# Optimization experiments

Measured on AMD Instinct MI355X. Metric: run time of the kernel, lower is better.

Reference implementation:

```python
import jax, jax.numpy as jnp
import numpy as np

B, S, D, H = 2, 4096, 128, 128
EPS = 1e-6
NEG_INF = -1e30


def _complex_linear(xr, xi, Wr, Wi, br, bi):
    # x: (B,S,D); W: (H,D); complex linear (Wr + i Wi)(xr + i xi) + (br + i bi) per layer math:
    # real_out = (xr Wr + br) - (xi Wi + bi); imag_out = (xi Wr + br) + (xr Wi + bi)
    out_r = xr @ Wr.T + br - (xi @ Wi.T + bi)
    out_i = xi @ Wr.T + br + (xr @ Wi.T + bi)
    return out_r, out_i


def setup_inputs() -> dict:
    key = jax.random.key(0)
    ks = jax.random.split(key, 24)
    scale = 1.0 / np.sqrt(D)
    def W(k):
        return jax.random.normal(k, (H, D), jnp.float32) * scale
    def b(k):
        return jax.random.normal(k, (H,), jnp.float32) * 0.01
    inp = {
        "Z_q": jax.random.normal(ks[0], (B, 2, S, D, 1), jnp.float32),
        "Z_k": jax.random.normal(ks[1], (B, 2, S, D, 1), jnp.float32),
        "Z_v": jax.random.normal(ks[2], (B, 2, S, D, 1), jnp.float32),
        "Wq_r": W(ks[3]), "Wq_i": W(ks[4]), "bq_r": b(ks[5]), "bq_i": b(ks[6]),
        "Wk_r": W(ks[7]), "Wk_i": W(ks[8]), "bk_r": b(ks[9]), "bk_i": b(ks[10]),
        "Wv_r": W(ks[11]), "Wv_i": W(ks[12]), "bv_r": b(ks[13]), "bv_i": b(ks[14]),
        "Wp_r": W(ks[15]), "Wp_i": W(ks[16]), "bp_r": b(ks[17]), "bp_i": b(ks[18]),
        "noise_floor": jnp.asarray(1.0, jnp.float32),
        "tau": jnp.asarray(0.0, jnp.float32),
    }
    return inp


def reference(Z_q, Z_k, Z_v,
              Wq_r, Wq_i, bq_r, bq_i,
              Wk_r, Wk_i, bk_r, bk_i,
              Wv_r, Wv_i, bv_r, bv_i,
              Wp_r, Wp_i, bp_r, bp_i,
              noise_floor, tau):
    # squeeze trailing singleton; split real/imag -> (B,S,D)
    zqr, zqi = Z_q[:, 0, :, :, 0], Z_q[:, 1, :, :, 0]
    zkr, zki = Z_k[:, 0, :, :, 0], Z_k[:, 1, :, :, 0]
    zvr, zvi = Z_v[:, 0, :, :, 0], Z_v[:, 1, :, :, 0]

    Qr, Qi = _complex_linear(zqr, zqi, Wq_r, Wq_i, bq_r, bq_i)
    Kr, Ki = _complex_linear(zkr, zki, Wk_r, Wk_i, bk_r, bk_i)
    Vr, Vi = _complex_linear(zvr, zvi, Wv_r, Wv_i, bv_r, bv_i)

    # InverseMahalanobis: R2[b,i,j] = sum_h |Q[b,i]-K[b,j]|^2
    q2 = jnp.sum(Qr * Qr + Qi * Qi, axis=-1)          # (B,S)
    k2 = jnp.sum(Kr * Kr + Ki * Ki, axis=-1)          # (B,S)
    re_qk = (jnp.einsum('bsh,bth->bst', Qr, Kr)
             + jnp.einsum('bsh,bth->bst', Qi, Ki))    # (B,S,S)
    R2 = q2[:, :, None] + k2[:, None, :] - 2.0 * re_qk

    attn_scores = -jax.nn.softplus(tau) * jnp.log(noise_floor ** 2 + R2 + EPS)
    mask = jnp.tril(jnp.ones((S, S), dtype=bool))[None]
    attn_scores = jnp.where(mask, attn_scores, NEG_INF)
    attn_weights = jax.nn.softmax(attn_scores / jnp.sqrt(jnp.float32(H)), axis=-1)

    # attn (real) times complex V
    est_r = jnp.einsum('bst,bth->bsh', attn_weights, Vr)
    est_i = jnp.einsum('bst,bth->bsh', attn_weights, Vi)

    out_r, out_i = _complex_linear(est_r, est_i, Wp_r, Wp_i, bp_r, bp_i)
    out = jnp.stack((out_r, out_i), axis=1)[..., None]  # (B,2,S,H,1)
    return out, attn_weights
```

## Files before the change

### kernel.cpp

```cpp
#include <hip/hip_runtime.h>

#define S_LEN 4096
#define OUT_ELEMS 2097152

typedef _Float16 f16;
typedef _Float16 f16x8 __attribute__((ext_vector_type(8)));
typedef _Float16 f16x4 __attribute__((ext_vector_type(4)));
typedef float f32x4 __attribute__((ext_vector_type(4)));

#define MT_OFF    0x000000
#define BIAS_OFF  0x080000
#define SC_OFF    0x081000
#define QH_OFF    0x100000
#define KH_OFF    0x500000
#define VH_OFF    0x900000
#define Q2_OFF    0xD00000
#define K2_OFF    0xD10000
#define L_OFF     0xD20000
#define VPT_OFF   0xE00000
#define PW_OFF    0x1600000
#define WS_NEED   0x5600000

#define MFMA16(A,B,C) __builtin_amdgcn_mfma_f32_16x16x32_f16(A,B,C,0,0,0)

__device__ __forceinline__ void async_cp16(f16* lds, const f16* g) {
  __builtin_amdgcn_global_load_lds(
      (const __attribute__((address_space(1))) void*)g,
      (__attribute__((address_space(3))) void*)lds, 16, 0, 0);
}


template<int LC>
__device__ __forceinline__ void stageT(f16* lds, const f16* g, size_t stride, int tid) {
#pragma unroll
  for (int i = 0; i < (1 << (LC - 1)); ++i) {
    int idx = i*256 + tid;
    int row = idx >> LC, c = idx & ((1 << LC) - 1);
    int cl = c ^ (row & 7);
    async_cp16(lds + idx*8, g + (size_t)row*stride + cl*8);
  }
}

template<int LC>
__device__ __forceinline__ void mfma_stepT(const f16* Asm, const f16* Bsm, int kb,
                                           int lane, int wm, int wn, f32x4 acc[4][4]) {
  f16x8 a[4], b[4];
  int rr = lane & 15, q = lane >> 4;
  int L = kb*4 + q;
#pragma unroll
  for (int i=0;i<4;i++) {
    int row = wm + i*16 + rr;
    a[i] = *(const f16x8*)(Asm + (row << (LC+3)) + ((L ^ (row & 7)) << 3));
  }
#pragma unroll
  for (int j=0;j<4;j++) {
    int row = wn + j*16 + rr;
    b[j] = *(const f16x8*)(Bsm + (row << (LC+3)) + ((L ^ (row & 7)) << 3));
  }
#pragma unroll
  for (int i=0;i<4;i++)
#pragma unroll
    for (int j=0;j<4;j++) acc[i][j] = MFMA16(a[i], b[j], acc[i][j]);
}

__device__ __forceinline__ void stage16(f16* lds, const f16* g, int stride, int tid) {
#pragma unroll
  for (int i = 0; i < 2; ++i) {
    int idx = i*256 + tid;
    int row = idx >> 2, c = idx & 3;
    int cs = c ^ ((row >> 1) & 3);
    async_cp16(lds + idx*8, g + (size_t)row*stride + cs*8);
  }
}

__device__ __forceinline__ void mfma_step(const f16* Asm, const f16* Bsm, int lane,
                                          int wm, int wn, f32x4 acc[4][4]) {
  f16x8 a[4], b[4];
  int rr = lane & 15;
  int sc = (lane >> 4) ^ ((rr >> 1) & 3);
#pragma unroll
  for (int i=0;i<4;i++) a[i] = *(const f16x8*)(Asm + (wm + i*16 + rr)*32 + (sc<<3));
#pragma unroll
  for (int j=0;j<4;j++) b[j] = *(const f16x8*)(Bsm + (wn + j*16 + rr)*32 + (sc<<3));
#pragma unroll
  for (int i=0;i<4;i++)
#pragma unroll
    for (int j=0;j<4;j++) acc[i][j] = MFMA16(a[i], b[j], acc[i][j]);
}

__global__ __launch_bounds__(256)
void k_build(const float* Wqr, const float* Wqi, const float* bqr, const float* bqi,
             const float* Wkr, const float* Wki, const float* bkr, const float* bki,
             const float* Wvr, const float* Wvi, const float* bvr, const float* bvi,
             const float* Wpr, const float* Wpi, const float* bpr, const float* bpi,
             f16* Mt, float* bias) {
  int mat = blockIdx.x;
  const float *Wr, *Wi, *br, *bi;
  if (mat == 0)      { Wr=Wqr; Wi=Wqi; br=bqr; bi=bqi; }
  else if (mat == 1) { Wr=Wkr; Wi=Wki; br=bkr; bi=bki; }
  else if (mat == 2) { Wr=Wvr; Wi=Wvi; br=bvr; bi=bvi; }
  else               { Wr=Wpr; Wi=Wpi; br=bpr; bi=bpi; }
  int idx = blockIdx.y*256 + threadIdx.x;
  int n = idx >> 8, k = idx & 255;
  int d = k & 127, h = n & 127;
  float w = (k < 128) ? ((n < 128) ? Wr[h*128+d] : Wi[h*128+d])
                      : ((n < 128) ? -Wi[h*128+d] : Wr[h*128+d]);
  Mt[mat*65536 + n*256 + k] = (f16)w;
  if (k == 0)
    bias[mat*256 + n] = (n < 128) ? (br[n] - bi[n]) : (br[n-128] + bi[n-128]);
}

__global__ __launch_bounds__(256)
void k_init(float* attn, float* zreg, float* sc, const float* nf, const float* tau) {
  int bx = blockIdx.x, tid = threadIdx.x;
  float4 z = make_float4(0.f,0.f,0.f,0.f);
  if (bx < 992) {
    int b = bx >= 496; int r = bx - b*496;
    int tb = 1; while (r >= tb) { r -= tb; tb++; }
    int sb = r;
    float* base = attn + ((size_t)(b*S_LEN) + sb*128)*S_LEN + tb*128;
    int c4 = tid & 31;
#pragma unroll
    for (int it = 0; it < 16; ++it) {
      int row = it*8 + (tid >> 5);
      *(float4*)(base + (size_t)row*S_LEN + c4*4) = z;
    }
    return;
  }
  int idx = (bx - 992)*256 + tid;
  if (idx < 12288) ((float4*)zreg)[idx] = z;
  if (idx == 0) {
    float t = tau[0];
    float c = __builtin_log2f(1.0f + __builtin_exp2f(t * 1.4426950408889634f))
              * 0.6931471805599453f;
    sc[0] = -c * 0.08838834764831845f;
    sc[1] = nf[0]*nf[0] + 1e-6f;
  }
}

__global__ __launch_bounds__(256)
void k_proj(const float* Zq, const float* Zk, const float* Zv,
            const f16* Mt, const float* bias,
            f16* Qh, f16* Kh, f16* Vh, float* q2, float* k2) {
  __shared__ f16 Asm[128*256];
  __shared__ f16 Bsm[128*256];
  __shared__ float bias_s[128];
  int tid = threadIdx.x;
  int mode = blockIdx.z;
  int m0 = blockIdx.x * 128, n0 = blockIdx.y * 128;
  const float* Z = (mode==0) ? Zq : (mode==1 ? Zk : Zv);
  if (tid < 128) bias_s[tid] = bias[mode*256 + n0 + tid];
  int b = m0 >> 12, s0 = m0 & 4095;
  stageT<5>(Bsm, Mt + mode*65536 + n0*256, 256, tid);
  const float* Zb = Z + ((size_t)(b*2))*S_LEN*128 + (size_t)s0*128;
#pragma unroll
  for (int i = 0; i < 32; ++i) {
    int idx = i*256 + tid;
    int row = idx >> 6, c4 = idx & 63;
    int part = c4 >> 5, d4 = c4 & 31;
    float4 v = *(const float4*)(Zb + ((size_t)part*S_LEN + row)*128 + d4*4);
    f16x4 hv; hv[0]=(f16)v.x; hv[1]=(f16)v.y; hv[2]=(f16)v.z; hv[3]=(f16)v.w;
    int ch = c4 >> 1;
    *(f16x4*)(Asm + (row << 8) + ((ch ^ (row & 7)) << 3) + (c4 & 1)*4) = hv;
  }
  __syncthreads();
  int lane = tid & 63, w = tid >> 6;
  int wm = (w >> 1)*64, wn = (w & 1)*64;
  f32x4 acc[4][4] = {};
#pragma unroll
  for (int kb = 0; kb < 8; ++kb) mfma_stepT<5>(Asm, Bsm, kb, lane, wm, wn, acc);
  int rr = (lane>>4)*4, cc = lane & 15;
  f16* O = (mode==0) ? Qh : (mode==1 ? Kh : Vh);
  float rs[4][4];
#pragma unroll
  for (int i=0;i<4;i++)
#pragma unroll
    for (int r=0;r<4;r++) rs[i][r]=0.f;
#pragma unroll
  for (int i=0;i<4;i++)
#pragma unroll
    for (int j=0;j<4;j++) {
      int cl = wn + j*16 + cc;
      int cg = n0 + cl;
      float bv = bias_s[cl];
#pragma unroll
      for (int r=0;r<4;r++) {
        int rg = m0 + wm + i*16 + rr + r;
        f16 hv = (f16)(acc[i][j][r] + bv);
        O[(size_t)rg*256 + cg] = hv;
        float fv = (float)hv;
        rs[i][r] += fv*fv;
      }
    }
  if (mode < 2) {
#pragma unroll
    for (int m=8;m>=1;m>>=1)
#pragma unroll
      for (int i=0;i<4;i++)
#pragma unroll
        for (int r=0;r<4;r++) rs[i][r] += __shfl_xor(rs[i][r], m, 64);
    if (cc == 0) {
      float* T = (mode==0) ? q2 : k2;
#pragma unroll
      for (int i=0;i<4;i++)
#pragma unroll
        for (int r=0;r<4;r++) {
          int rg = m0 + wm + i*16 + rr + r;
          atomicAdd(&T[rg], rs[i][r]);
        }
    }
  }
}

__global__ __launch_bounds__(256)
void k_vp(const f16* Vh, const f16* Mt, f16* VPt) {
  __shared__ f16 Asm[2][128*32];
  __shared__ f16 Bsm[2][128*32];
  int t0 = blockIdx.x*128, n0 = blockIdx.y*128, b = blockIdx.z;
  int tid = threadIdx.x;
  int lane = tid & 63, w = tid >> 6;
  int wm = (w>>1)*64, wn = (w&1)*64;
  const f16* Ag = Mt + 3*65536 + n0*256;
  const f16* Bg = Vh + ((size_t)(b*S_LEN) + t0)*256;
  f32x4 acc[4][4] = {};
  stage16(Asm[0], Ag, 256, tid);
  stage16(Bsm[0], Bg, 256, tid);
  __syncthreads();
  for (int kb=0;kb<8;kb++) {
    int cur = kb & 1;
    if (kb < 7) {
      stage16(Asm[cur^1], Ag + (kb+1)*32, 256, tid);
      stage16(Bsm[cur^1], Bg + (kb+1)*32, 256, tid);
    }
    mfma_step(Asm[cur], Bsm[cur], lane, wm, wn, acc);
    __syncthreads();
  }
  int rr = (lane>>4)*4, cc = lane & 15;
#pragma unroll
  for (int i=0;i<4;i++) {
    int n = n0 + wm + i*16 + rr;
#pragma unroll
    for (int j=0;j<4;j++) {
      int t = t0 + wn + j*16 + cc;
#pragma unroll
      for (int r=0;r<4;r++)
        VPt[(size_t)b*1048576 + (size_t)(n + r)*4096 + t] = (f16)acc[i][j][r];
    }
  }
}

__global__ __launch_bounds__(256)
void k_attn(const f16* Qh, const f16* Kh, const float* q2, const float* k2,
            const float* sc, float* lsum, f16* Pws) {
  __shared__ f16 Qs[128*256];
  __shared__ f16 Ks[128*256];
  __shared__ float q2s[128], k2s[128];
  int x = blockIdx.x;
  int b = x >= 528; int r = x - b*528;
  int sb = 0; while (r > sb) { r -= sb + 1; sb++; }
  int tb = r;
  int s0 = sb*128, t0 = tb*128;
  int tid = threadIdx.x;
  stageT<5>(Qs, Qh + ((size_t)(b*S_LEN) + s0)*256, 256, tid);
  stageT<5>(Ks, Kh + ((size_t)(b*S_LEN) + t0)*256, 256, tid);
  if (tid < 128) {
    q2s[tid] = q2[b*S_LEN + s0 + tid];
    k2s[tid] = k2[b*S_LEN + t0 + tid];
  }
  __syncthreads();
  float kc = sc[0], nf2 = sc[1];
  int lane = tid & 63, w = tid >> 6;
  int wm = (w >> 1)*64, wn = (w & 1)*64;
  f32x4 acc[4][4] = {};
#pragma unroll
  for (int kb = 0; kb < 8; ++kb) mfma_stepT<5>(Qs, Ks, kb, lane, wm, wn, acc);
  int rr = (lane>>4)*4, cc = lane & 15;
  bool diag = (tb == sb);
  float rs[4][4];
#pragma unroll
  for (int i=0;i<4;i++)
#pragma unroll
    for (int rg=0;rg<4;rg++) rs[i][rg]=0.f;
#pragma unroll
  for (int i=0;i<4;i++)
#pragma unroll
    for (int j=0;j<4;j++) {
      int cl = wn + j*16 + cc;
      float kv = k2s[cl];
#pragma unroll
      for (int rg=0;rg<4;rg++) {
        int rl = wm + i*16 + rr + rg;
        float xx = nf2 + q2s[rl] + kv - 2.0f*acc[i][j][rg];
        float P = __builtin_exp2f(kc * __builtin_log2f(__builtin_fmaxf(xx, 1e-6f)));
        if (diag && (t0+cl) > (s0+rl)) P = 0.f;
        Pws[((size_t)(b*S_LEN) + s0 + rl)*S_LEN + t0 + cl] = (f16)P;
        rs[i][rg] += P;
      }
    }
#pragma unroll
  for (int m=8;m>=1;m>>=1)
#pragma unroll
    for (int i=0;i<4;i++)
#pragma unroll
      for (int rg=0;rg<4;rg++) rs[i][rg] += __shfl_xor(rs[i][rg], m, 64);
  if (cc == 0)
#pragma unroll
    for (int i=0;i<4;i++)
#pragma unroll
      for (int rg=0;rg<4;rg++) {
        int rl = wm + i*16 + rr + rg;
        atomicAdd(&lsum[b*S_LEN + s0 + rl], rs[i][rg]);
      }
}

__global__ __launch_bounds__(256)
void k_pv(const f16* Pws, const f16* VPt, const float* lsum, const float* bias,
          float* outp, float* attn) {
  __shared__ f16 Asm[2][128*128];
  __shared__ f16 Bsm[2][128*128];
  __shared__ float ls[128];
  __shared__ float bias_s[128];
  int sb = blockIdx.x, nb = blockIdx.y, b = blockIdx.z;
  int s0 = sb*128, h0 = nb*128;
  int nt = sb + 1;
  int tid = threadIdx.x;
  bool wrb = (nb == 0);
  if (tid < 128) {
    ls[tid] = 1.0f / lsum[b*S_LEN + s0 + tid];
    bias_s[tid] = bias[3*256 + h0 + tid];
  }
  const f16* Abase = Pws + ((size_t)(b*S_LEN) + s0)*S_LEN;
  const f16* Bbase = VPt + (size_t)b*1048576 + (size_t)h0*4096;
  stageT<4>(Asm[0], Abase, S_LEN, tid);
  stageT<4>(Bsm[0], Bbase, 4096, tid);
  __syncthreads();
  int lane = tid & 63, w = tid >> 6;
  int wm = (w>>1)*64, wn = (w&1)*64;
  f32x4 acc[4][4] = {};
  for (int t = 0; t < nt; ++t) {
    int cur = t & 1;
    if (t + 1 < nt) {
      stageT<4>(Asm[cur^1], Abase + (t+1)*128, S_LEN, tid);
      stageT<4>(Bsm[cur^1], Bbase + (t+1)*128, 4096, tid);
    }
    if (wrb) {
      int c4 = tid & 31;
#pragma unroll
      for (int i = 0; i < 16; ++i) {
        int idx = i*256 + tid;
        int row = idx >> 5;
        float invl = ls[row];
        f16x4 v = *(const f16x4*)(Asm[cur] + (row << 7)
                                  + (((c4 >> 1) ^ (row & 7)) << 3) + (c4 & 1)*4);
        float4 o;
        o.x=(float)v[0]*invl; o.y=(float)v[1]*invl; o.z=(float)v[2]*invl; o.w=(float)v[3]*invl;
        *(float4*)(attn + ((size_t)(b*S_LEN) + s0 + row)*S_LEN + t*128 + c4*4) = o;
      }
    }
#pragma unroll
    for (int kb = 0; kb < 4; ++kb) mfma_stepT<4>(Asm[cur], Bsm[cur], kb, lane, wm, wn, acc);
    __syncthreads();
  }
  int rr = (lane>>4)*4, cc = lane & 15;
#pragma unroll
  for (int i=0;i<4;i++)
#pragma unroll
    for (int j=0;j<4;j++) {
      int cl = wn + j*16 + cc;
      int cg = h0 + cl;
      int comp = cg >> 7, h = cg & 127;
      float bv = bias_s[cl];
#pragma unroll
      for (int rg=0;rg<4;rg++) {
        int rl = wm + i*16 + rr + rg;
        outp[(((size_t)(b*2 + comp))*S_LEN + s0 + rl)*128 + h] = acc[i][j][rg]*ls[rl] + bv;
      }
    }
}

extern "C" void kernel_launch(void* const* d_in, const int* in_sizes, int n_in,
                              void* d_out, int out_size, void* d_ws, size_t ws_size,
                              hipStream_t stream) {
  (void)in_sizes; (void)n_in; (void)out_size;
  if (ws_size < (size_t)WS_NEED) return;
  const float* Zq = (const float*)d_in[0];
  const float* Zk = (const float*)d_in[1];
  const float* Zv = (const float*)d_in[2];
  char* ws = (char*)d_ws;
  f16*   Mt   = (f16*)(ws + MT_OFF);
  float* bias = (float*)(ws + BIAS_OFF);
  float* sc   = (float*)(ws + SC_OFF);
  f16*   Qh   = (f16*)(ws + QH_OFF);
  f16*   Kh   = (f16*)(ws + KH_OFF);
  f16*   Vh   = (f16*)(ws + VH_OFF);
  float* q2   = (float*)(ws + Q2_OFF);
  float* k2   = (float*)(ws + K2_OFF);
  float* lsum = (float*)(ws + L_OFF);
  f16*   VPt  = (f16*)(ws + VPT_OFF);
  f16*   Pws  = (f16*)(ws + PW_OFF);
  float* outp = (float*)d_out;
  float* attn = outp + OUT_ELEMS;

  k_build<<<dim3(4,256), 256, 0, stream>>>(
      (const float*)d_in[3],  (const float*)d_in[4],  (const float*)d_in[5],  (const float*)d_in[6],
      (const float*)d_in[7],  (const float*)d_in[8],  (const float*)d_in[9],  (const float*)d_in[10],
      (const float*)d_in[11], (const float*)d_in[12], (const float*)d_in[13], (const float*)d_in[14],
      (const float*)d_in[15], (const float*)d_in[16], (const float*)d_in[17], (const float*)d_in[18],
      Mt, bias);
  k_init<<<1040, 256, 0, stream>>>(attn, q2, sc, (const float*)d_in[19], (const float*)d_in[20]);
  k_proj<<<dim3(64,2,3), 256, 0, stream>>>(Zq, Zk, Zv, Mt, bias, Qh, Kh, Vh, q2, k2);
  k_vp<<<dim3(32,2,2), 256, 0, stream>>>(Vh, Mt, VPt);
  k_attn<<<1056, 256, 0, stream>>>(Qh, Kh, q2, k2, sc, lsum, Pws);
  k_pv<<<dim3(32,2,2), 256, 0, stream>>>(Pws, VPt, lsum, bias, outp, attn);
}
```

Before: 343.5 us.

## Recompute attention probabilities in PV kernel instead of materializing them

The fp16 probability matrix is no longer written to workspace. A new k_lsum kernel computes only the row sums of the scores. k_pv recomputes the Q·K scores per key block, writes the normalized attention output, and multiplies by VP in a split-K layout over groups of up to four key blocks. Outputs are accumulated with atomics onto an output buffer that k_init now pre-fills with the bias. The projection epilogue also stages results through LDS so the global stores are coalesced. This removes a large round trip of the intermediate matrix and raises the block count in the PV stage, at the cost of computing QK twice and adding float atomics.

After: 402.6 us. 1.17x slower.

```diff
diff --git a/kernel.cpp b/kernel.cpp
--- a/kernel.cpp
+++ b/kernel.cpp
@@ -18,7 +18,6 @@
 #define K2_OFF    0xD10000
 #define L_OFF     0xD20000
 #define VPT_OFF   0xE00000
-#define PW_OFF    0x1600000
 #define WS_NEED   0x5600000
 
 #define MFMA16(A,B,C) __builtin_amdgcn_mfma_f32_16x16x32_f16(A,B,C,0,0,0)
@@ -111,7 +110,8 @@
 }
 
 __global__ __launch_bounds__(256)
-void k_init(float* attn, float* zreg, float* sc, const float* nf, const float* tau) {
+void k_init(float* outp, float* attn, float* zreg, float* sc, const float* bias,
+            const float* nf, const float* tau) {
   int bx = blockIdx.x, tid = threadIdx.x;
   float4 z = make_float4(0.f,0.f,0.f,0.f);
   if (bx < 992) {
@@ -128,7 +128,14 @@
     return;
   }
   int idx = (bx - 992)*256 + tid;
-  if (idx < 12288) ((float4*)zreg)[idx] = z;
+  if (idx < 524288) {
+    int h4 = idx & 31;
+    int comp = (idx >> 17) & 1;
+    ((float4*)outp)[idx] = *(const float4*)(bias + 3*256 + comp*128 + h4*4);
+  } else {
+    int j = idx - 524288;
+    if (j < 12288) ((float4*)zreg)[j] = z;
+  }
   if (idx == 0) {
     float t = tau[0];
     float c = __builtin_log2f(1.0f + __builtin_exp2f(t * 1.4426950408889634f))
@@ -169,8 +176,10 @@
   f32x4 acc[4][4] = {};
 #pragma unroll
   for (int kb = 0; kb < 8; ++kb) mfma_stepT<5>(Asm, Bsm, kb, lane, wm, wn, acc);
-  int rr = (lane>>4)*4, cc = lane & 15;
+  int rr2 = (lane>>4)*4, cc = lane & 15;
   f16* O = (mode==0) ? Qh : (mode==1 ? Kh : Vh);
+  __syncthreads();
+  f16* Osm = Asm;
   float rs[4][4];
 #pragma unroll
   for (int i=0;i<4;i++)
@@ -181,17 +190,23 @@
 #pragma unroll
     for (int j=0;j<4;j++) {
       int cl = wn + j*16 + cc;
-      int cg = n0 + cl;
       float bv = bias_s[cl];
 #pragma unroll
       for (int r=0;r<4;r++) {
-        int rg = m0 + wm + i*16 + rr + r;
+        int rl = wm + i*16 + rr2 + r;
         f16 hv = (f16)(acc[i][j][r] + bv);
-        O[(size_t)rg*256 + cg] = hv;
+        Osm[rl*128 + cl] = hv;
         float fv = (float)hv;
         rs[i][r] += fv*fv;
       }
     }
+  __syncthreads();
+#pragma unroll
+  for (int i2 = 0; i2 < 8; ++i2) {
+    int idx = i2*256 + tid;
+    int row = idx >> 4, c = idx & 15;
+    *(f16x8*)(O + (size_t)(m0+row)*256 + n0 + c*8) = *(const f16x8*)(Osm + row*128 + c*8);
+  }
   if (mode < 2) {
 #pragma unroll
     for (int m=8;m>=1;m>>=1)
@@ -205,7 +220,7 @@
       for (int i=0;i<4;i++)
 #pragma unroll
         for (int r=0;r<4;r++) {
-          int rg = m0 + wm + i*16 + rr + r;
+          int rg = m0 + wm + i*16 + rr2 + r;
           atomicAdd(&T[rg], rs[i][r]);
         }
     }
@@ -235,10 +250,10 @@
     mfma_step(Asm[cur], Bsm[cur], lane, wm, wn, acc);
     __syncthreads();
   }
-  int rr = (lane>>4)*4, cc = lane & 15;
+  int rr2 = (lane>>4)*4, cc = lane & 15;
 #pragma unroll
   for (int i=0;i<4;i++) {
-    int n = n0 + wm + i*16 + rr;
+    int n = n0 + wm + i*16 + rr2;
 #pragma unroll
     for (int j=0;j<4;j++) {
       int t = t0 + wn + j*16 + cc;
@@ -249,9 +264,9 @@
   }
 }
 
-__global__ __launch_bounds__(256)
-void k_attn(const f16* Qh, const f16* Kh, const float* q2, const float* k2,
-            const float* sc, float* lsum, f16* Pws) {
+__global__ __launch_bounds__(512, 2)
+void k_lsum(const f16* Qh, const f16* Kh, const float* q2, const float* k2,
+            const float* sc, float* lsum) {
   __shared__ f16 Qs[128*256];
   __shared__ f16 Ks[128*256];
   __shared__ float q2s[128], k2s[128];
@@ -261,20 +276,35 @@
   int tb = r;
   int s0 = sb*128, t0 = tb*128;
   int tid = threadIdx.x;
-  stageT<5>(Qs, Qh + ((size_t)(b*S_LEN) + s0)*256, 256, tid);
-  stageT<5>(Ks, Kh + ((size_t)(b*S_LEN) + t0)*256, 256, tid);
-  if (tid < 128) {
-    q2s[tid] = q2[b*S_LEN + s0 + tid];
-    k2s[tid] = k2[b*S_LEN + t0 + tid];
-  }
+  const f16* Qg = Qh + ((size_t)(b*S_LEN) + s0)*256;
+  const f16* Kg = Kh + ((size_t)(b*S_LEN) + t0)*256;
+#pragma unroll
+  for (int i=0;i<8;i++) {
+    int idx = i*512 + tid, row = idx >> 5, c = idx & 31, cl = c ^ (row & 7);
+    async_cp16(Qs + idx*8, Qg + (size_t)row*256 + cl*8);
+    async_cp16(Ks + idx*8, Kg + (size_t)row*256 + cl*8);
+  }
+  if (tid < 128) { q2s[tid]=q2[b*S_LEN+s0+tid]; k2s[tid]=k2[b*S_LEN+t0+tid]; }
   __syncthreads();
   float kc = sc[0], nf2 = sc[1];
   int lane = tid & 63, w = tid >> 6;
-  int wm = (w >> 1)*64, wn = (w & 1)*64;
-  f32x4 acc[4][4] = {};
-#pragma unroll
-  for (int kb = 0; kb < 8; ++kb) mfma_stepT<5>(Qs, Ks, kb, lane, wm, wn, acc);
-  int rr = (lane>>4)*4, cc = lane & 15;
+  int wm = (w>>2)*64, wn = (w&3)*32;
+  int rr = lane & 15, qq = lane >> 4;
+  f32x4 acc[4][2] = {};
+#pragma unroll
+  for (int kb=0;kb<8;kb++) {
+    int L = kb*4 + qq;
+    f16x8 a[4], bb[2];
+#pragma unroll
+    for (int i=0;i<4;i++){ int row=wm+i*16+rr; a[i]=*(const f16x8*)(Qs + row*256 + ((L^(row&7))<<3)); }
+#pragma unroll
+    for (int j=0;j<2;j++){ int row=wn+j*16+rr; bb[j]=*(const f16x8*)(Ks + row*256 + ((L^(row&7))<<3)); }
+#pragma unroll
+    for (int i=0;i<4;i++)
+#pragma unroll
+      for (int j=0;j<2;j++) acc[i][j]=MFMA16(a[i],bb[j],acc[i][j]);
+  }
+  int rr2 = qq*4, cc = rr;
   bool diag = (tb == sb);
   float rs[4][4];
 #pragma unroll
@@ -284,16 +314,15 @@
 #pragma unroll
   for (int i=0;i<4;i++)
 #pragma unroll
-    for (int j=0;j<4;j++) {
+    for (int j=0;j<2;j++) {
       int cl = wn + j*16 + cc;
       float kv = k2s[cl];
 #pragma unroll
       for (int rg=0;rg<4;rg++) {
-        int rl = wm + i*16 + rr + rg;
+        int rl = wm + i*16 + rr2 + rg;
         float xx = nf2 + q2s[rl] + kv - 2.0f*acc[i][j][rg];
         float P = __builtin_exp2f(kc * __builtin_log2f(__builtin_fmaxf(xx, 1e-6f)));
         if (diag && (t0+cl) > (s0+rl)) P = 0.f;
-        Pws[((size_t)(b*S_LEN) + s0 + rl)*S_LEN + t0 + cl] = (f16)P;
         rs[i][rg] += P;
       }
     }
@@ -307,73 +336,152 @@
 #pragma unroll
     for (int i=0;i<4;i++)
 #pragma unroll
+      for (int rg=0;rg<4;rg++)
+        atomicAdd(&lsum[b*S_LEN + s0 + wm + i*16 + rr2 + rg], rs[i][rg]);
+}
+
+__global__ __launch_bounds__(512, 2)
+void k_pv(const f16* Qh, const f16* Kh, const f16* VPt,
+          const float* q2, const float* k2, const float* sc,
+          const float* lsum, float* outp, float* attn) {
+  __shared__ f16 Qs[128*256];
+  __shared__ f16 KPV[128*256];
+  int r = blockIdx.x, b = blockIdx.y;
+  int sb = 0; while (r >= ((sb+4)>>2)) { r -= (sb+4)>>2; sb++; }
+  int c = r;
+  int s0 = sb*128;
+  int tid = threadIdx.x;
+  int lane = tid & 63, w = tid >> 6;
+  int wm = (w>>2)*64;
+  int wnq = (w&3)*32;
+  int wnp = (w&3)*64;
+  int rr = lane & 15, qq = lane >> 4, rr2 = qq*4, cc = rr;
+  const f16* Qg = Qh + ((size_t)(b*S_LEN) + s0)*256;
+#pragma unroll
+  for (int i=0;i<8;i++) {
+    int idx = i*512 + tid, row = idx >> 5, ch = idx & 31, cl = ch ^ (row & 7);
+    async_cp16(Qs + idx*8, Qg + (size_t)row*256 + cl*8);
+  }
+  float kc = sc[0], nf2 = sc[1];
+  float q2v[4][4], lsr[4][4];
+#pragma unroll
+  for (int i=0;i<4;i++) {
+    float4 qv = *(const float4*)(q2  + b*S_LEN + s0 + wm + i*16 + rr2);
+    float4 lv = *(const float4*)(lsum + b*S_LEN + s0 + wm + i*16 + rr2);
+    q2v[i][0]=qv.x; q2v[i][1]=qv.y; q2v[i][2]=qv.z; q2v[i][3]=qv.w;
+    lsr[i][0]=1.0f/lv.x; lsr[i][1]=1.0f/lv.y; lsr[i][2]=1.0f/lv.z; lsr[i][3]=1.0f/lv.w;
+  }
+  float invl[8];
+#pragma unroll
+  for (int i=0;i<8;i++) { int row=(i*512+tid)>>5; invl[i]=1.0f/lsum[b*S_LEN+s0+row]; }
+  const f16* VPg = VPt + (size_t)b*1048576;
+  f32x4 pacc[4][4] = {};
+  int tb0 = c*4, tb1 = tb0 + 4; if (tb1 > sb+1) tb1 = sb+1;
+  for (int tb = tb0; tb < tb1; ++tb) {
+    int t0 = tb*128;
+    bool diag = (tb == sb);
+    __syncthreads();
+    const f16* Kg = Kh + ((size_t)(b*S_LEN) + t0)*256;
+#pragma unroll
+    for (int i=0;i<8;i++) {
+      int idx = i*512 + tid, row = idx >> 5, ch = idx & 31, cl = ch ^ (row & 7);
+      async_cp16(KPV + idx*8, Kg + (size_t)row*256 + cl*8);
+    }
+    __syncthreads();
+    f32x4 qacc[4][2] = {};
+#pragma unroll
+    for (int kb=0;kb<8;kb++) {
+      int L = kb*4 + qq;
+      f16x8 a[4], bb[2];
+#pragma unroll
+      for (int i=0;i<4;i++){ int row=wm+i*16+rr; a[i]=*(const f16x8*)(Qs + row*256 + ((L^(row&7))<<3)); }
+#pragma unroll
+      for (int j=0;j<2;j++){ int row=wnq+j*16+rr; bb[j]=*(const f16x8*)(KPV + row*256 + ((L^(row&7))<<3)); }
+#pragma unroll
+      for (int i=0;i<4;i++)
+#pragma unroll
+        for (int j=0;j<2;j++) qacc[i][j]=MFMA16(a[i],bb[j],qacc[i][j]);
+    }
+    __syncthreads();
+#pragma unroll
+    for (int i=0;i<4;i++) {
+      int idx = i*512 + tid, row = idx >> 3, ch = idx & 7, cl = ch ^ (row & 7);
+      async_cp16(KPV + 16384 + idx*8, VPg + (size_t)row*4096 + t0 + cl*8);
+    }
+    float kv2[2];
+#pragma unroll
+    for (int j=0;j<2;j++) kv2[j] = k2[b*S_LEN + t0 + wnq + j*16 + cc];
+#pragma unroll
+    for (int i=0;i<4;i++)
+#pragma unroll
+      for (int j=0;j<2;j++) {
+        int cl = wnq + j*16 + cc;
+#pragma unroll
+        for (int rg=0;rg<4;rg++) {
+          int rl = wm + i*16 + rr2 + rg;
+          float xx = nf2 + q2v[i][rg] + kv2[j] - 2.0f*qacc[i][j][rg];
+          float P = __builtin_exp2f(kc * __builtin_log2f(__builtin_fmaxf(xx, 1e-6f)));
+          if (diag && (t0+cl) > (s0+rl)) P = 0.f;
+          int ch = cl >> 3;
+          KPV[rl*128 + ((ch ^ (rl&7)) << 3) + (cl & 7)] = (f16)P;
+        }
+      }
+    __syncthreads();
+#pragma unroll
+    for (int i2=0;i2<8;i2++) {
+      int idx = i2*512 + tid, row = idx >> 5, c4 = idx & 31;
+      f16x4 v = *(const f16x4*)(KPV + row*128 + (((c4>>1) ^ (row&7)) << 3) + (c4&1)*4);
+      float4 o;
+      o.x=(float)v[0]*invl[i2]; o.y=(float)v[1]*invl[i2];
+      o.z=(float)v[2]*invl[i2]; o.w=(float)v[3]*invl[i2];
+      *(float4*)(attn + ((size_t)(b*S_LEN) + s0 + row)*S_LEN + t0 + c4*4) = o;
+    }
+#pragma unroll
+    for (int kk=0;kk<2;kk++) {
+      int Lp = kk*4 + qq;
+      f16x8 a[4], bb[4];
+#pragma unroll
+      for (int i=0;i<4;i++){ int row=wm+i*16+rr; a[i]=*(const f16x8*)(KPV + row*128 + ((Lp^(row&7))<<3)); }
+#pragma unroll
+      for (int j=0;j<4;j++){ int rv=wnp+j*16+rr; bb[j]=*(const f16x8*)(KPV + 16384 + rv*64 + ((Lp^(rv&7))<<3)); }
+#pragma unroll
+      for (int i=0;i<4;i++)
+#pragma unroll
+        for (int j=0;j<4;j++) pacc[i][j]=MFMA16(a[i],bb[j],pacc[i][j]);
+    }
+    __syncthreads();
+#pragma unroll
+    for (int i=0;i<4;i++) {
+      int idx = i*512 + tid, row = idx >> 3, ch = idx & 7, cl = ch ^ (row & 7);
+      async_cp16(KPV + 16384 + idx*8, VPg + (size_t)row*4096 + t0 + 64 + cl*8);
+    }
+    __syncthreads();
+#pragma unroll
+    for (int kk=0;kk<2;kk++) {
+      int Lp = 8 + kk*4 + qq;
+      int Lv = kk*4 + qq;
+      f16x8 a[4], bb[4];
+#pragma unroll
+      for (int i=0;i<4;i++){ int row=wm+i*16+rr; a[i]=*(const f16x8*)(KPV + row*128 + ((Lp^(row&7))<<3)); }
+#pragma unroll
+      for (int j=0;j<4;j++){ int rv=wnp+j*16+rr; bb[j]=*(const f16x8*)(KPV + 16384 + rv*64 + ((Lv^(rv&7))<<3)); }
+#pragma unroll
+      for (int i=0;i<4;i++)
+#pragma unroll
+        for (int j=0;j<4;j++) pacc[i][j]=MFMA16(a[i],bb[j],pacc[i][j]);
+    }
+  }
+#pragma unroll
+  for (int i=0;i<4;i++)
+#pragma unroll
+    for (int j=0;j<4;j++) {
+      int cg = wnp + j*16 + cc;
+      int comp = cg >> 7, h = cg & 127;
+#pragma unroll
       for (int rg=0;rg<4;rg++) {
-        int rl = wm + i*16 + rr + rg;
-        atomicAdd(&lsum[b*S_LEN + s0 + rl], rs[i][rg]);
-      }
-}
-
-__global__ __launch_bounds__(256)
-void k_pv(const f16* Pws, const f16* VPt, const float* lsum, const float* bias,
-          float* outp, float* attn) {
-  __shared__ f16 Asm[2][128*128];
-  __shared__ f16 Bsm[2][128*128];
-  __shared__ float ls[128];
-  __shared__ float bias_s[128];
-  int sb = blockIdx.x, nb = blockIdx.y, b = blockIdx.z;
-  int s0 = sb*128, h0 = nb*128;
-  int nt = sb + 1;
-  int tid = threadIdx.x;
-  bool wrb = (nb == 0);
-  if (tid < 128) {
-    ls[tid] = 1.0f / lsum[b*S_LEN + s0 + tid];
-    bias_s[tid] = bias[3*256 + h0 + tid];
-  }
-  const f16* Abase = Pws + ((size_t)(b*S_LEN) + s0)*S_LEN;
-  const f16* Bbase = VPt + (size_t)b*1048576 + (size_t)h0*4096;
-  stageT<4>(Asm[0], Abase, S_LEN, tid);
-  stageT<4>(Bsm[0], Bbase, 4096, tid);
-  __syncthreads();
-  int lane = tid & 63, w = tid >> 6;
-  int wm = (w>>1)*64, wn = (w&1)*64;
-  f32x4 acc[4][4] = {};
-  for (int t = 0; t < nt; ++t) {
-    int cur = t & 1;
-    if (t + 1 < nt) {
-      stageT<4>(Asm[cur^1], Abase + (t+1)*128, S_LEN, tid);
-      stageT<4>(Bsm[cur^1], Bbase + (t+1)*128, 4096, tid);
-    }
-    if (wrb) {
-      int c4 = tid & 31;
-#pragma unroll
-      for (int i = 0; i < 16; ++i) {
-        int idx = i*256 + tid;
-        int row = idx >> 5;
-        float invl = ls[row];
-        f16x4 v = *(const f16x4*)(Asm[cur] + (row << 7)
-                                  + (((c4 >> 1) ^ (row & 7)) << 3) + (c4 & 1)*4);
-        float4 o;
-        o.x=(float)v[0]*invl; o.y=(float)v[1]*invl; o.z=(float)v[2]*invl; o.w=(float)v[3]*invl;
-        *(float4*)(attn + ((size_t)(b*S_LEN) + s0 + row)*S_LEN + t*128 + c4*4) = o;
-      }
-    }
-#pragma unroll
-    for (int kb = 0; kb < 4; ++kb) mfma_stepT<4>(Asm[cur], Bsm[cur], kb, lane, wm, wn, acc);
-    __syncthreads();
-  }
-  int rr = (lane>>4)*4, cc = lane & 15;
-#pragma unroll
-  for (int i=0;i<4;i++)
-#pragma unroll
-    for (int j=0;j<4;j++) {
-      int cl = wn + j*16 + cc;
-      int cg = h0 + cl;
-      int comp = cg >> 7, h = cg & 127;
-      float bv = bias_s[cl];
-#pragma unroll
-      for (int rg=0;rg<4;rg++) {
-        int rl = wm + i*16 + rr + rg;
-        outp[(((size_t)(b*2 + comp))*S_LEN + s0 + rl)*128 + h] = acc[i][j][rg]*ls[rl] + bv;
+        int rl = wm + i*16 + rr2 + rg;
+        atomicAdd(&outp[(((size_t)(b*2 + comp))*S_LEN + s0 + rl)*128 + h],
+                  pacc[i][j][rg]*lsr[i][rg]);
       }
     }
 }
@@ -397,7 +505,6 @@
   float* k2   = (float*)(ws + K2_OFF);
   float* lsum = (float*)(ws + L_OFF);
   f16*   VPt  = (f16*)(ws + VPT_OFF);
-  f16*   Pws  = (f16*)(ws + PW_OFF);
   float* outp = (float*)d_out;
   float* attn = outp + OUT_ELEMS;
 
@@ -407,9 +514,10 @@
       (const float*)d_in[11], (const float*)d_in[12], (const float*)d_in[13], (const float*)d_in[14],
       (const float*)d_in[15], (const float*)d_in[16], (const float*)d_in[17], (const float*)d_in[18],
       Mt, bias);
-  k_init<<<1040, 256, 0, stream>>>(attn, q2, sc, (const float*)d_in[19], (const float*)d_in[20]);
+  k_init<<<3088, 256, 0, stream>>>(outp, attn, q2, sc, bias,
+                                   (const float*)d_in[19], (const float*)d_in[20]);
   k_proj<<<dim3(64,2,3), 256, 0, stream>>>(Zq, Zk, Zv, Mt, bias, Qh, Kh, Vh, q2, k2);
   k_vp<<<dim3(32,2,2), 256, 0, stream>>>(Vh, Mt, VPt);
-  k_attn<<<1056, 256, 0, stream>>>(Qh, Kh, q2, k2, sc, lsum, Pws);
-  k_pv<<<dim3(32,2,2), 256, 0, stream>>>(Pws, VPt, lsum, bias, outp, attn);
-}
+  k_lsum<<<1056, 512, 0, stream>>>(Qh, Kh, q2, k2, sc, lsum);
+  k_pv<<<dim3(144,2), 512, 0, stream>>>(Qh, Kh, VPt, q2, k2, sc, lsum, outp, attn);
+}
```
